# Kernel optimization log

Measured on AMD Instinct MI355X. Metric: run time of the kernel, lower is better.

Reference implementation:

```python
import jax, jax.numpy as jnp
import numpy as np

B, S, D = 2, 2048, 1024
H, E = 16, 64


def setup_inputs() -> dict:
    key = jax.random.key(0)
    k1, k2, k3, k4 = jax.random.split(key, 4)
    x = jax.random.normal(k1, (B, S, D), dtype=jnp.float32)
    # per-head Q/K/V projection weights, stacked over the head axis
    scale = 1.0 / np.sqrt(D)
    Wq = jax.random.normal(k2, (H, D, E), dtype=jnp.float32) * scale
    Wk = jax.random.normal(k3, (H, D, E), dtype=jnp.float32) * scale
    Wv = jax.random.normal(k4, (H, D, E), dtype=jnp.float32) * scale
    return {"x": x, "Wq": Wq, "Wk": Wk, "Wv": Wv}


def reference(x, Wq, Wk, Wv):
    # Grouped-over-heads equivalent of the per-head torch loop.
    q = jnp.einsum("bsd,hde->bhse", x, Wq)  # [B,H,S,E]
    k = jnp.einsum("bsd,hde->bhse", x, Wk)
    v = jnp.einsum("bsd,hde->bhse", x, Wv)

    scores = jnp.einsum("bhse,bhte->bhst", q, k)  # [B,H,S,S]
    scores = scores / jnp.sqrt(jnp.asarray(E, dtype=scores.dtype))
    causal = jnp.tril(jnp.ones((S, S), dtype=bool))  # True on/below diagonal
    scores = jnp.where(causal, scores, jnp.finfo(scores.dtype).min)
    attn = jax.nn.softmax(scores, axis=-1)  # dropout p=0.0 -> identity

    out = jnp.einsum("bhst,bhte->bhse", attn, v)  # [B,H,S,E]
    # concat over heads on the last dim, matching torch.concat(..., dim=-1)
    return out.transpose(0, 2, 1, 3).reshape(B, S, H * E)
```

## Files before the change

### kernel.cpp

```cpp
#include <hip/hip_runtime.h>
#include <stdint.h>

#define S_LEN 2048
#define D_DIM 1024
#define NB 2
#define NH 16
#define NE 64
#define M_ROWS (NB * S_LEN)
#define N_COLS (3 * NH * NE)
#define K_DIM D_DIM

typedef unsigned short u16;
typedef unsigned int u32;
typedef u16 u16x8 __attribute__((ext_vector_type(8)));
typedef __bf16 bf16x8 __attribute__((ext_vector_type(8)));
typedef float f32x4 __attribute__((ext_vector_type(4)));

__device__ __forceinline__ u16 f2b(float f) {
  u32 u = __builtin_bit_cast(u32, f);
  return (u16)((u + 0x7FFFu + ((u >> 16) & 1u)) >> 16);
}

__device__ __forceinline__ void gload_lds16(const void* g, void* l) {
  __builtin_amdgcn_global_load_lds(
      (const __attribute__((address_space(1))) u32*)g,
      (__attribute__((address_space(3))) u32*)l, 16, 0, 0);
}

__global__ __launch_bounds__(256) void k_prep_x(const float* __restrict__ x,
                                                u16* __restrict__ xb) {
  size_t t = (size_t)blockIdx.x * 256 + threadIdx.x;
  const float4* xf = (const float4*)x;
  float4 a = xf[2 * t], c = xf[2 * t + 1];
  u16x8 o;
  o[0] = f2b(a.x); o[1] = f2b(a.y); o[2] = f2b(a.z); o[3] = f2b(a.w);
  o[4] = f2b(c.x); o[5] = f2b(c.y); o[6] = f2b(c.z); o[7] = f2b(c.w);
  *(u16x8*)(xb + 8 * t) = o;
}

__global__ __launch_bounds__(256) void k_prep_w(const float* __restrict__ Wq,
                                                const float* __restrict__ Wk,
                                                const float* __restrict__ Wv,
                                                u16* __restrict__ Wt) {
  __shared__ u16 tile[64][65];
  int bid = blockIdx.x;
  int kb = bid & 15;
  int h = (bid >> 4) & 15;
  int proj = bid >> 8;
  const float* W = (proj == 0) ? Wq : ((proj == 1) ? Wk : Wv);
  int k0 = kb * 64;
  int t = threadIdx.x;
  int e = t & 63, kr = t >> 6;
  const float* src = W + ((size_t)h * D_DIM + k0 + kr * 16) * NE + e;
#pragma unroll
  for (int j = 0; j < 16; ++j) tile[kr * 16 + j][e] = f2b(src[(size_t)j * NE]);
  __syncthreads();
  int e2 = t >> 2, kc = (t & 3) * 16;
  u16x8 o0, o1;
#pragma unroll
  for (int j = 0; j < 8; ++j) { o0[j] = tile[kc + j][e2]; o1[j] = tile[kc + 8 + j][e2]; }
  size_t n = (size_t)proj * 1024 + h * 64 + e2;
  u16* dst = Wt + n * K_DIM + k0 + kc;
  *(u16x8*)dst = o0;
  *(u16x8*)(dst + 8) = o1;
}

__global__ __launch_bounds__(256) void k_gemm(const u16* __restrict__ A,
                                              const u16* __restrict__ Bt,
                                              u16* __restrict__ C) {
  __shared__ __align__(16) u16 As[128 * 64];
  __shared__ __align__(16) u16 Bs[128 * 64];
  int t = threadIdx.x;
  int lane = t & 63, w = t >> 6;
  int wr = (w >> 1) * 64, wc = (w & 1) * 64;
  int m0 = blockIdx.x * 128, n0 = blockIdx.y * 128;
  float qscale = ((n0 + wc) < 1024) ? 0.18033688f : 1.0f;
  f32x4 acc[4][4];
#pragma unroll
  for (int m = 0; m < 4; m++)
#pragma unroll
    for (int n = 0; n < 4; n++)
#pragma unroll
      for (int j = 0; j < 4; j++) acc[m][n][j] = 0.f;

  for (int k0 = 0; k0 < K_DIM; k0 += 64) {
#pragma unroll
    for (int i = 0; i < 4; ++i) {
      int ci = i * 256 + t;
      int row = ci >> 3, c = ci & 7;
      int cs = c ^ (row & 7);
      gload_lds16(A + (size_t)(m0 + row) * K_DIM + k0 + cs * 8,
                  (char*)As + (size_t)(i * 256 + w * 64) * 16);
      gload_lds16(Bt + (size_t)(n0 + row) * K_DIM + k0 + cs * 8,
                  (char*)Bs + (size_t)(i * 256 + w * 64) * 16);
    }
    __syncthreads();
#pragma unroll
    for (int ks = 0; ks < 2; ++ks) {
      int kc = ks * 4 + (lane >> 4);
      bf16x8 af[4], bfr[4];
#pragma unroll
      for (int m = 0; m < 4; m++) {
        int r = wr + m * 16 + (lane & 15);
        af[m] = *(const bf16x8*)&As[r * 64 + ((kc ^ (r & 7)) * 8)];
      }
#pragma unroll
      for (int n = 0; n < 4; n++) {
        int r = wc + n * 16 + (lane & 15);
        bfr[n] = *(const bf16x8*)&Bs[r * 64 + ((kc ^ (r & 7)) * 8)];
      }
#pragma unroll
      for (int m = 0; m < 4; m++)
#pragma unroll
        for (int n = 0; n < 4; n++)
          acc[m][n] = __builtin_amdgcn_mfma_f32_16x16x32_bf16(af[m], bfr[n], acc[m][n], 0, 0, 0);
    }
    __syncthreads();
  }
#pragma unroll
  for (int m = 0; m < 4; m++) {
#pragma unroll
    for (int r = 0; r < 4; r++) {
      int row = m0 + wr + m * 16 + (lane >> 4) * 4 + r;
#pragma unroll
      for (int n = 0; n < 4; n++) {
        int col = n0 + wc + n * 16 + (lane & 15);
        C[(size_t)row * N_COLS + col] = f2b(acc[m][n][r] * qscale);
      }
    }
  }
}

__device__ __forceinline__ void stage_k(const u16* kb_, u16* kdst, int kv0, int t, int w) {
#pragma unroll
  for (int i = 0; i < 2; ++i) {
    int ci = i * 256 + t;
    int row = ci >> 3, c = ci & 7;
    int cs = c ^ (row & 7);
    gload_lds16(kb_ + (size_t)(kv0 + row) * N_COLS + cs * 8,
                (char*)kdst + (size_t)(i * 256 + w * 64) * 16);
  }
}

__device__ __forceinline__ void vwrite(u16* vt, u16x8 va, u16x8 vb2, int vp, int vec) {
#pragma unroll
  for (int j = 0; j < 8; ++j) {
    int e = vec * 8 + j;
    int slot = (vp >> 2) ^ (e & 7) ^ (e >> 3);
    *(u32*)((char*)vt + e * 128 + slot * 16 + (vp & 3) * 4) =
        (u32)va[j] | ((u32)vb2[j] << 16);
  }
}

__global__ __launch_bounds__(256) void k_attn(const u16* __restrict__ qkv,
                                              float* __restrict__ out) {
  __shared__ __align__(16) u16 Ks[2][64 * 64];
  __shared__ __align__(16) u16 Vt[2][64 * 64];
  __shared__ __align__(16) u16 Ps[64 * 64];
  int t = threadIdx.x;
  int lane = t & 63, w = t >> 6;
  int bid = blockIdx.x;
  int x = bid & 7, g = bid >> 3;
  int bh = x * 4 + (g & 3);
  int qt = 31 - (g >> 2);
  int b = bh >> 4, h = bh & 15;
  const u16* qb_ = qkv + (size_t)b * S_LEN * N_COLS + h * NE;
  const u16* kb_ = qb_ + 1024;
  const u16* vb_ = qb_ + 2048;
  int vp = t >> 3, vec = t & 7;

  int q0 = qt * 64;
  int nt = qt + 1;

  int qrow = q0 + w * 16 + (lane & 15);
  bf16x8 qf[2];
#pragma unroll
  for (int ks = 0; ks < 2; ks++)
    qf[ks] = *(const bf16x8*)(qb_ + (size_t)qrow * N_COLS + ks * 32 + (lane >> 4) * 8);

  f32x4 o[4];
#pragma unroll
  for (int i = 0; i < 4; i++)
#pragma unroll
    for (int j = 0; j < 4; j++) o[i][j] = 0.f;
  float lrow[4];
#pragma unroll
  for (int r = 0; r < 4; r++) lrow[r] = 0.f;
  int myq = q0 + w * 16 + (lane >> 4) * 4;

  stage_k(kb_, Ks[0], 0, t, w);
  {
    const u16* vs = vb_ + (size_t)(2 * vp) * N_COLS + vec * 8;
    u16x8 va = *(const u16x8*)vs;
    u16x8 vb2 = *(const u16x8*)(vs + N_COLS);
    vwrite(Vt[0], va, vb2, vp, vec);
  }
  __syncthreads();

  int cur = 0;
  for (int ti = 0; ti < nt; ++ti) {
    int kv0 = ti * 64;
    bool pf = (ti + 1 < nt);
    u16x8 va, vb2;
    if (pf) {
      const u16* vs = vb_ + (size_t)(kv0 + 64 + 2 * vp) * N_COLS + vec * 8;
      va = *(const u16x8*)vs;
      vb2 = *(const u16x8*)(vs + N_COLS);
      stage_k(kb_, Ks[cur ^ 1], kv0 + 64, t, w);
    }

    f32x4 s[4];
#pragma unroll
    for (int f = 0; f < 4; f++)
#pragma unroll
      for (int j = 0; j < 4; j++) s[f][j] = 0.f;
    __builtin_amdgcn_s_setprio(1);
#pragma unroll
    for (int ks = 0; ks < 2; ks++) {
      int kc = ks * 4 + (lane >> 4);
#pragma unroll
      for (int f = 0; f < 4; f++) {
        int r = f * 16 + (lane & 15);
        bf16x8 kf = *(const bf16x8*)&Ks[cur][r * 64 + ((kc ^ (r & 7)) * 8)];
        s[f] = __builtin_amdgcn_mfma_f32_16x16x32_bf16(qf[ks], kf, s[f], 0, 0, 0);
      }
    }
    __builtin_amdgcn_s_setprio(0);

    bool diag = (ti == nt - 1);
#pragma unroll
    for (int r = 0; r < 4; ++r) {
#pragma unroll
      for (int f = 0; f < 4; f++) {
        float p = __builtin_amdgcn_exp2f(s[f][r]);
        if (diag) {
          int kv = kv0 + f * 16 + (lane & 15);
          p = (kv <= myq + r) ? p : 0.f;
        }
        s[f][r] = p;
      }
      lrow[r] += (s[0][r] + s[1][r]) + (s[2][r] + s[3][r]);
    }

#pragma unroll
    for (int f = 0; f < 4; f++) {
#pragma unroll
      for (int r = 0; r < 4; r++) {
        int row = w * 16 + (lane >> 4) * 4 + r;
        int col = f * 16 + (lane & 15);
        int swz = (col >> 3) ^ (row & 7);
        *(u16*)((char*)Ps + row * 128 + swz * 16 + (col & 7) * 2) =
            __builtin_bit_cast(u16, (__bf16)s[f][r]);
      }
    }

    if (pf) vwrite(Vt[cur ^ 1], va, vb2, vp, vec);

    __builtin_amdgcn_s_setprio(1);
#pragma unroll
    for (int ks = 0; ks < 2; ks++) {
      int kc = ks * 4 + (lane >> 4);
      int pr = w * 16 + (lane & 15);
      bf16x8 pa = *(const bf16x8*)&Ps[pr * 64 + ((kc ^ (pr & 7)) * 8)];
#pragma unroll
      for (int ef = 0; ef < 4; ef++) {
        int vr = ef * 16 + (lane & 15);
        int vswz = kc ^ (vr & 7) ^ (vr >> 3);
        bf16x8 vbf = *(const bf16x8*)&Vt[cur][vr * 64 + vswz * 8];
        o[ef] = __builtin_amdgcn_mfma_f32_16x16x32_bf16(pa, vbf, o[ef], 0, 0, 0);
      }
    }
    __builtin_amdgcn_s_setprio(0);
    __syncthreads();
    cur ^= 1;
  }

#pragma unroll
  for (int r = 0; r < 4; r++) {
    float l = lrow[r];
    l += __shfl_xor(l, 1);
    l += __shfl_xor(l, 2);
    l += __shfl_xor(l, 4);
    l += __shfl_xor(l, 8);
    float inv = 1.0f / l;
    int q = myq + r;
#pragma unroll
    for (int ef = 0; ef < 4; ef++) {
      int col = h * NE + ef * 16 + (lane & 15);
      out[((size_t)b * S_LEN + q) * (NH * NE) + col] = o[ef][r] * inv;
    }
  }
}

extern "C" void kernel_launch(void* const* d_in, const int* in_sizes, int n_in,
                              void* d_out, int out_size, void* d_ws, size_t ws_size,
                              hipStream_t stream) {
  const float* x = (const float*)d_in[0];
  const float* Wq = (const float*)d_in[1];
  const float* Wk = (const float*)d_in[2];
  const float* Wv = (const float*)d_in[3];
  float* out = (float*)d_out;

  char* ws = (char*)d_ws;
  u16* xb = (u16*)ws;
  u16* Wt = (u16*)(ws + (8u << 20));
  u16* qkv = (u16*)(ws + (14u << 20));

  k_prep_x<<<dim3(2048), dim3(256), 0, stream>>>(x, xb);
  k_prep_w<<<dim3(768), dim3(256), 0, stream>>>(Wq, Wk, Wv, Wt);
  k_gemm<<<dim3(32, 24), dim3(256), 0, stream>>>(xb, Wt, qkv);
  k_attn<<<dim3(1024), dim3(256), 0, stream>>>(qkv, out);
}
```

Baseline: 98.19 us.

## Merge prep kernels, remap GEMM blocks per XCD, use 128-row query tiles

Merges the x and weight conversion kernels into one launch to remove a kernel boundary. Remaps the GEMM grid to 1D so each XCD works on a contiguous group of column tiles, aiming for better L2 reuse of the weights. The attention kernel grows to 512 threads with 128 query rows per block, so each K/V tile staged in shared memory serves twice as many queries. Only the first 256 threads load V, and the last two KV tiles are masked. This halves the attention grid and may lower occupancy or leave load imbalance across the causal blocks.

Measured after the change: 100.3 us. +2.1%, slower.

```diff
diff --git a/kernel.cpp b/kernel.cpp
--- a/kernel.cpp
+++ b/kernel.cpp
@@ -27,42 +27,44 @@
       (__attribute__((address_space(3))) u32*)l, 16, 0, 0);
 }
 
-__global__ __launch_bounds__(256) void k_prep_x(const float* __restrict__ x,
-                                                u16* __restrict__ xb) {
-  size_t t = (size_t)blockIdx.x * 256 + threadIdx.x;
-  const float4* xf = (const float4*)x;
-  float4 a = xf[2 * t], c = xf[2 * t + 1];
-  u16x8 o;
-  o[0] = f2b(a.x); o[1] = f2b(a.y); o[2] = f2b(a.z); o[3] = f2b(a.w);
-  o[4] = f2b(c.x); o[5] = f2b(c.y); o[6] = f2b(c.z); o[7] = f2b(c.w);
-  *(u16x8*)(xb + 8 * t) = o;
-}
-
-__global__ __launch_bounds__(256) void k_prep_w(const float* __restrict__ Wq,
-                                                const float* __restrict__ Wk,
-                                                const float* __restrict__ Wv,
-                                                u16* __restrict__ Wt) {
+__global__ __launch_bounds__(256) void k_prep(const float* __restrict__ x,
+                                              const float* __restrict__ Wq,
+                                              const float* __restrict__ Wk,
+                                              const float* __restrict__ Wv,
+                                              u16* __restrict__ xb,
+                                              u16* __restrict__ Wt) {
   __shared__ u16 tile[64][65];
   int bid = blockIdx.x;
-  int kb = bid & 15;
-  int h = (bid >> 4) & 15;
-  int proj = bid >> 8;
-  const float* W = (proj == 0) ? Wq : ((proj == 1) ? Wk : Wv);
-  int k0 = kb * 64;
   int t = threadIdx.x;
-  int e = t & 63, kr = t >> 6;
-  const float* src = W + ((size_t)h * D_DIM + k0 + kr * 16) * NE + e;
-#pragma unroll
-  for (int j = 0; j < 16; ++j) tile[kr * 16 + j][e] = f2b(src[(size_t)j * NE]);
-  __syncthreads();
-  int e2 = t >> 2, kc = (t & 3) * 16;
-  u16x8 o0, o1;
-#pragma unroll
-  for (int j = 0; j < 8; ++j) { o0[j] = tile[kc + j][e2]; o1[j] = tile[kc + 8 + j][e2]; }
-  size_t n = (size_t)proj * 1024 + h * 64 + e2;
-  u16* dst = Wt + n * K_DIM + k0 + kc;
-  *(u16x8*)dst = o0;
-  *(u16x8*)(dst + 8) = o1;
+  if (bid < 2048) {
+    size_t i = (size_t)bid * 256 + t;
+    const float4* xf = (const float4*)x;
+    float4 a = xf[2 * i], c = xf[2 * i + 1];
+    u16x8 o;
+    o[0] = f2b(a.x); o[1] = f2b(a.y); o[2] = f2b(a.z); o[3] = f2b(a.w);
+    o[4] = f2b(c.x); o[5] = f2b(c.y); o[6] = f2b(c.z); o[7] = f2b(c.w);
+    *(u16x8*)(xb + 8 * i) = o;
+  } else {
+    int wbid = bid - 2048;
+    int kb = wbid & 15;
+    int h = (wbid >> 4) & 15;
+    int proj = wbid >> 8;
+    const float* W = (proj == 0) ? Wq : ((proj == 1) ? Wk : Wv);
+    int k0 = kb * 64;
+    int e = t & 63, kr = t >> 6;
+    const float* src = W + ((size_t)h * D_DIM + k0 + kr * 16) * NE + e;
+#pragma unroll
+    for (int j = 0; j < 16; ++j) tile[kr * 16 + j][e] = f2b(src[(size_t)j * NE]);
+    __syncthreads();
+    int e2 = t >> 2, kc = (t & 3) * 16;
+    u16x8 o0, o1;
+#pragma unroll
+    for (int j = 0; j < 8; ++j) { o0[j] = tile[kc + j][e2]; o1[j] = tile[kc + 8 + j][e2]; }
+    size_t n = (size_t)proj * 1024 + h * 64 + e2;
+    u16* dst = Wt + n * K_DIM + k0 + kc;
+    *(u16x8*)dst = o0;
+    *(u16x8*)(dst + 8) = o1;
+  }
 }
 
 __global__ __launch_bounds__(256) void k_gemm(const u16* __restrict__ A,
@@ -73,7 +75,10 @@
   int t = threadIdx.x;
   int lane = t & 63, w = t >> 6;
   int wr = (w >> 1) * 64, wc = (w & 1) * 64;
-  int m0 = blockIdx.x * 128, n0 = blockIdx.y * 128;
+  int bid = blockIdx.x;
+  int xcd = bid & 7, r0 = bid >> 3;
+  int m0 = (r0 / 3) * 128;
+  int n0 = (xcd * 3 + (r0 % 3)) * 128;
   float qscale = ((n0 + wc) < 1024) ? 0.18033688f : 1.0f;
   f32x4 acc[4][4];
 #pragma unroll
@@ -131,15 +136,11 @@
   }
 }
 
-__device__ __forceinline__ void stage_k(const u16* kb_, u16* kdst, int kv0, int t, int w) {
-#pragma unroll
-  for (int i = 0; i < 2; ++i) {
-    int ci = i * 256 + t;
-    int row = ci >> 3, c = ci & 7;
-    int cs = c ^ (row & 7);
-    gload_lds16(kb_ + (size_t)(kv0 + row) * N_COLS + cs * 8,
-                (char*)kdst + (size_t)(i * 256 + w * 64) * 16);
-  }
+__device__ __forceinline__ void stage_k(const u16* kb_, u16* kdst, int kv0, int t) {
+  int row = t >> 3, c = t & 7;
+  int cs = c ^ (row & 7);
+  gload_lds16(kb_ + (size_t)(kv0 + row) * N_COLS + cs * 8,
+              (char*)kdst + (size_t)t * 16);
 }
 
 __device__ __forceinline__ void vwrite(u16* vt, u16x8 va, u16x8 vb2, int vp, int vec) {
@@ -152,25 +153,25 @@
   }
 }
 
-__global__ __launch_bounds__(256) void k_attn(const u16* __restrict__ qkv,
+__global__ __launch_bounds__(512) void k_attn(const u16* __restrict__ qkv,
                                               float* __restrict__ out) {
   __shared__ __align__(16) u16 Ks[2][64 * 64];
   __shared__ __align__(16) u16 Vt[2][64 * 64];
-  __shared__ __align__(16) u16 Ps[64 * 64];
+  __shared__ __align__(16) u16 Ps[128 * 64];
   int t = threadIdx.x;
   int lane = t & 63, w = t >> 6;
   int bid = blockIdx.x;
-  int x = bid & 7, g = bid >> 3;
-  int bh = x * 4 + (g & 3);
-  int qt = 31 - (g >> 2);
+  int xcd = bid & 7, g = bid >> 3;
+  int bh = xcd * 4 + (g & 3);
+  int qb = 15 - (g >> 2);
   int b = bh >> 4, h = bh & 15;
   const u16* qb_ = qkv + (size_t)b * S_LEN * N_COLS + h * NE;
   const u16* kb_ = qb_ + 1024;
   const u16* vb_ = qb_ + 2048;
   int vp = t >> 3, vec = t & 7;
 
-  int q0 = qt * 64;
-  int nt = qt + 1;
+  int q0 = qb * 128;
+  int nt = 2 * qb + 2;
 
   int qrow = q0 + w * 16 + (lane & 15);
   bf16x8 qf[2];
@@ -188,8 +189,8 @@
   for (int r = 0; r < 4; r++) lrow[r] = 0.f;
   int myq = q0 + w * 16 + (lane >> 4) * 4;
 
-  stage_k(kb_, Ks[0], 0, t, w);
-  {
+  stage_k(kb_, Ks[0], 0, t);
+  if (t < 256) {
     const u16* vs = vb_ + (size_t)(2 * vp) * N_COLS + vec * 8;
     u16x8 va = *(const u16x8*)vs;
     u16x8 vb2 = *(const u16x8*)(vs + N_COLS);
@@ -203,10 +204,12 @@
     bool pf = (ti + 1 < nt);
     u16x8 va, vb2;
     if (pf) {
-      const u16* vs = vb_ + (size_t)(kv0 + 64 + 2 * vp) * N_COLS + vec * 8;
-      va = *(const u16x8*)vs;
-      vb2 = *(const u16x8*)(vs + N_COLS);
-      stage_k(kb_, Ks[cur ^ 1], kv0 + 64, t, w);
+      if (t < 256) {
+        const u16* vs = vb_ + (size_t)(kv0 + 64 + 2 * vp) * N_COLS + vec * 8;
+        va = *(const u16x8*)vs;
+        vb2 = *(const u16x8*)(vs + N_COLS);
+      }
+      stage_k(kb_, Ks[cur ^ 1], kv0 + 64, t);
     }
 
     f32x4 s[4];
@@ -227,13 +230,13 @@
     }
     __builtin_amdgcn_s_setprio(0);
 
-    bool diag = (ti == nt - 1);
+    bool mask = (ti >= nt - 2);
 #pragma unroll
     for (int r = 0; r < 4; ++r) {
 #pragma unroll
       for (int f = 0; f < 4; f++) {
         float p = __builtin_amdgcn_exp2f(s[f][r]);
-        if (diag) {
+        if (mask) {
           int kv = kv0 + f * 16 + (lane & 15);
           p = (kv <= myq + r) ? p : 0.f;
         }
@@ -254,7 +257,7 @@
       }
     }
 
-    if (pf) vwrite(Vt[cur ^ 1], va, vb2, vp, vec);
+    if (pf && t < 256) vwrite(Vt[cur ^ 1], va, vb2, vp, vec);
 
     __builtin_amdgcn_s_setprio(1);
 #pragma unroll
@@ -306,8 +309,7 @@
   u16* Wt = (u16*)(ws + (8u << 20));
   u16* qkv = (u16*)(ws + (14u << 20));
 
-  k_prep_x<<<dim3(2048), dim3(256), 0, stream>>>(x, xb);
-  k_prep_w<<<dim3(768), dim3(256), 0, stream>>>(Wq, Wk, Wv, Wt);
-  k_gemm<<<dim3(32, 24), dim3(256), 0, stream>>>(xb, Wt, qkv);
-  k_attn<<<dim3(1024), dim3(256), 0, stream>>>(qkv, out);
-}
+  k_prep<<<dim3(2816), dim3(256), 0, stream>>>(x, Wq, Wk, Wv, xb, Wt);
+  k_gemm<<<dim3(768), dim3(256), 0, stream>>>(xb, Wt, qkv);
+  k_attn<<<dim3(512), dim3(512), 0, stream>>>(qkv, out);
+}
```

## Merge prep kernels, remap GEMM blocks per XCD, keep P in registers

Applied to the files above, without the earlier changes.

Combines the x-conversion and weight-transpose kernels into one launch, which removes one kernel launch. Remaps GEMM blocks to a 1D grid so each XCD gets a contiguous set of N tiles, aiming for better L2 reuse. In attention it swaps the MFMA operand order so S comes out transposed, which lets P feed the PV MFMA straight from registers without the shared-memory round trip. The V fragments are then read as two 8-byte LDS loads, and the row-sum reduction changes to match. The extra LDS reads for V and the shuffle-based normalisation add some cost.

Measured after the change: 93.92 us. 1.05x faster.

```diff
diff --git a/kernel.cpp b/kernel.cpp
--- a/kernel.cpp
+++ b/kernel.cpp
@@ -6,7 +6,6 @@
 #define NB 2
 #define NH 16
 #define NE 64
-#define M_ROWS (NB * S_LEN)
 #define N_COLS (3 * NH * NE)
 #define K_DIM D_DIM
 
@@ -14,6 +13,7 @@
 typedef unsigned int u32;
 typedef u16 u16x8 __attribute__((ext_vector_type(8)));
 typedef __bf16 bf16x8 __attribute__((ext_vector_type(8)));
+typedef __bf16 bf16x4 __attribute__((ext_vector_type(4)));
 typedef float f32x4 __attribute__((ext_vector_type(4)));
 
 __device__ __forceinline__ u16 f2b(float f) {
@@ -27,42 +27,44 @@
       (__attribute__((address_space(3))) u32*)l, 16, 0, 0);
 }
 
-__global__ __launch_bounds__(256) void k_prep_x(const float* __restrict__ x,
-                                                u16* __restrict__ xb) {
-  size_t t = (size_t)blockIdx.x * 256 + threadIdx.x;
-  const float4* xf = (const float4*)x;
-  float4 a = xf[2 * t], c = xf[2 * t + 1];
-  u16x8 o;
-  o[0] = f2b(a.x); o[1] = f2b(a.y); o[2] = f2b(a.z); o[3] = f2b(a.w);
-  o[4] = f2b(c.x); o[5] = f2b(c.y); o[6] = f2b(c.z); o[7] = f2b(c.w);
-  *(u16x8*)(xb + 8 * t) = o;
-}
-
-__global__ __launch_bounds__(256) void k_prep_w(const float* __restrict__ Wq,
-                                                const float* __restrict__ Wk,
-                                                const float* __restrict__ Wv,
-                                                u16* __restrict__ Wt) {
+__global__ __launch_bounds__(256) void k_prep(const float* __restrict__ x,
+                                              const float* __restrict__ Wq,
+                                              const float* __restrict__ Wk,
+                                              const float* __restrict__ Wv,
+                                              u16* __restrict__ xb,
+                                              u16* __restrict__ Wt) {
   __shared__ u16 tile[64][65];
   int bid = blockIdx.x;
-  int kb = bid & 15;
-  int h = (bid >> 4) & 15;
-  int proj = bid >> 8;
-  const float* W = (proj == 0) ? Wq : ((proj == 1) ? Wk : Wv);
-  int k0 = kb * 64;
   int t = threadIdx.x;
-  int e = t & 63, kr = t >> 6;
-  const float* src = W + ((size_t)h * D_DIM + k0 + kr * 16) * NE + e;
-#pragma unroll
-  for (int j = 0; j < 16; ++j) tile[kr * 16 + j][e] = f2b(src[(size_t)j * NE]);
-  __syncthreads();
-  int e2 = t >> 2, kc = (t & 3) * 16;
-  u16x8 o0, o1;
-#pragma unroll
-  for (int j = 0; j < 8; ++j) { o0[j] = tile[kc + j][e2]; o1[j] = tile[kc + 8 + j][e2]; }
-  size_t n = (size_t)proj * 1024 + h * 64 + e2;
-  u16* dst = Wt + n * K_DIM + k0 + kc;
-  *(u16x8*)dst = o0;
-  *(u16x8*)(dst + 8) = o1;
+  if (bid < 2048) {
+    size_t i = (size_t)bid * 256 + t;
+    const float4* xf = (const float4*)x;
+    float4 a = xf[2 * i], c = xf[2 * i + 1];
+    u16x8 o;
+    o[0] = f2b(a.x); o[1] = f2b(a.y); o[2] = f2b(a.z); o[3] = f2b(a.w);
+    o[4] = f2b(c.x); o[5] = f2b(c.y); o[6] = f2b(c.z); o[7] = f2b(c.w);
+    *(u16x8*)(xb + 8 * i) = o;
+  } else {
+    int wbid = bid - 2048;
+    int kb = wbid & 15;
+    int h = (wbid >> 4) & 15;
+    int proj = wbid >> 8;
+    const float* W = (proj == 0) ? Wq : ((proj == 1) ? Wk : Wv);
+    int k0 = kb * 64;
+    int e = t & 63, kr = t >> 6;
+    const float* src = W + ((size_t)h * D_DIM + k0 + kr * 16) * NE + e;
+#pragma unroll
+    for (int j = 0; j < 16; ++j) tile[kr * 16 + j][e] = f2b(src[(size_t)j * NE]);
+    __syncthreads();
+    int e2 = t >> 2, kc = (t & 3) * 16;
+    u16x8 o0, o1;
+#pragma unroll
+    for (int j = 0; j < 8; ++j) { o0[j] = tile[kc + j][e2]; o1[j] = tile[kc + 8 + j][e2]; }
+    size_t n = (size_t)proj * 1024 + h * 64 + e2;
+    u16* dst = Wt + n * K_DIM + k0 + kc;
+    *(u16x8*)dst = o0;
+    *(u16x8*)(dst + 8) = o1;
+  }
 }
 
 __global__ __launch_bounds__(256) void k_gemm(const u16* __restrict__ A,
@@ -73,7 +75,10 @@
   int t = threadIdx.x;
   int lane = t & 63, w = t >> 6;
   int wr = (w >> 1) * 64, wc = (w & 1) * 64;
-  int m0 = blockIdx.x * 128, n0 = blockIdx.y * 128;
+  int bid = blockIdx.x;
+  int xcd = bid & 7, r0 = bid >> 3;
+  int m0 = (r0 / 3) * 128;
+  int n0 = (xcd * 3 + (r0 % 3)) * 128;
   float qscale = ((n0 + wc) < 1024) ? 0.18033688f : 1.0f;
   f32x4 acc[4][4];
 #pragma unroll
@@ -156,9 +161,9 @@
                                               float* __restrict__ out) {
   __shared__ __align__(16) u16 Ks[2][64 * 64];
   __shared__ __align__(16) u16 Vt[2][64 * 64];
-  __shared__ __align__(16) u16 Ps[64 * 64];
   int t = threadIdx.x;
   int lane = t & 63, w = t >> 6;
+  int hi = lane >> 4, l15 = lane & 15;
   int bid = blockIdx.x;
   int x = bid & 7, g = bid >> 3;
   int bh = x * 4 + (g & 3);
@@ -171,22 +176,20 @@
 
   int q0 = qt * 64;
   int nt = qt + 1;
-
-  int qrow = q0 + w * 16 + (lane & 15);
+  int wqb = q0 + w * 16;
+
   bf16x8 qf[2];
 #pragma unroll
   for (int ks = 0; ks < 2; ks++)
-    qf[ks] = *(const bf16x8*)(qb_ + (size_t)qrow * N_COLS + ks * 32 + (lane >> 4) * 8);
+    qf[ks] = *(const bf16x8*)(qb_ + (size_t)(wqb + l15) * N_COLS + ks * 32 + hi * 8);
 
   f32x4 o[4];
 #pragma unroll
   for (int i = 0; i < 4; i++)
 #pragma unroll
     for (int j = 0; j < 4; j++) o[i][j] = 0.f;
-  float lrow[4];
-#pragma unroll
-  for (int r = 0; r < 4; r++) lrow[r] = 0.f;
-  int myq = q0 + w * 16 + (lane >> 4) * 4;
+  float lsum = 0.f;
+  int myq = wqb + l15;
 
   stage_k(kb_, Ks[0], 0, t, w);
   {
@@ -217,40 +220,28 @@
     __builtin_amdgcn_s_setprio(1);
 #pragma unroll
     for (int ks = 0; ks < 2; ks++) {
-      int kc = ks * 4 + (lane >> 4);
+      int kc = ks * 4 + hi;
 #pragma unroll
       for (int f = 0; f < 4; f++) {
-        int r = f * 16 + (lane & 15);
+        int r = f * 16 + l15;
         bf16x8 kf = *(const bf16x8*)&Ks[cur][r * 64 + ((kc ^ (r & 7)) * 8)];
-        s[f] = __builtin_amdgcn_mfma_f32_16x16x32_bf16(qf[ks], kf, s[f], 0, 0, 0);
+        s[f] = __builtin_amdgcn_mfma_f32_16x16x32_bf16(kf, qf[ks], s[f], 0, 0, 0);
       }
     }
     __builtin_amdgcn_s_setprio(0);
 
     bool diag = (ti == nt - 1);
 #pragma unroll
-    for (int r = 0; r < 4; ++r) {
-#pragma unroll
-      for (int f = 0; f < 4; f++) {
+    for (int f = 0; f < 4; f++) {
+#pragma unroll
+      for (int r = 0; r < 4; r++) {
         float p = __builtin_amdgcn_exp2f(s[f][r]);
         if (diag) {
-          int kv = kv0 + f * 16 + (lane & 15);
-          p = (kv <= myq + r) ? p : 0.f;
+          int kv = kv0 + f * 16 + 4 * hi + r;
+          p = (kv <= myq) ? p : 0.f;
         }
         s[f][r] = p;
-      }
-      lrow[r] += (s[0][r] + s[1][r]) + (s[2][r] + s[3][r]);
-    }
-
-#pragma unroll
-    for (int f = 0; f < 4; f++) {
-#pragma unroll
-      for (int r = 0; r < 4; r++) {
-        int row = w * 16 + (lane >> 4) * 4 + r;
-        int col = f * 16 + (lane & 15);
-        int swz = (col >> 3) ^ (row & 7);
-        *(u16*)((char*)Ps + row * 128 + swz * 16 + (col & 7) * 2) =
-            __builtin_bit_cast(u16, (__bf16)s[f][r]);
+        lsum += p;
       }
     }
 
@@ -259,14 +250,25 @@
     __builtin_amdgcn_s_setprio(1);
 #pragma unroll
     for (int ks = 0; ks < 2; ks++) {
-      int kc = ks * 4 + (lane >> 4);
-      int pr = w * 16 + (lane & 15);
-      bf16x8 pa = *(const bf16x8*)&Ps[pr * 64 + ((kc ^ (pr & 7)) * 8)];
+      bf16x8 pa;
+#pragma unroll
+      for (int j = 0; j < 4; j++) {
+        pa[j] = (__bf16)s[2 * ks][j];
+        pa[4 + j] = (__bf16)s[2 * ks + 1][j];
+      }
+      int kvo1 = 32 * ks + 4 * hi;
+      int kvo2 = kvo1 + 16;
 #pragma unroll
       for (int ef = 0; ef < 4; ef++) {
-        int vr = ef * 16 + (lane & 15);
-        int vswz = kc ^ (vr & 7) ^ (vr >> 3);
-        bf16x8 vbf = *(const bf16x8*)&Vt[cur][vr * 64 + vswz * 8];
+        int e = ef * 16 + l15;
+        int sw = (e & 7) ^ (e >> 3);
+        int a1 = e * 128 + (((kvo1 >> 3) ^ sw) * 16) + (kvo1 & 7) * 2;
+        int a2 = e * 128 + (((kvo2 >> 3) ^ sw) * 16) + (kvo2 & 7) * 2;
+        bf16x4 vlo = *(const bf16x4*)((const char*)Vt[cur] + a1);
+        bf16x4 vhi = *(const bf16x4*)((const char*)Vt[cur] + a2);
+        bf16x8 vbf;
+#pragma unroll
+        for (int j = 0; j < 4; j++) { vbf[j] = vlo[j]; vbf[4 + j] = vhi[j]; }
         o[ef] = __builtin_amdgcn_mfma_f32_16x16x32_bf16(pa, vbf, o[ef], 0, 0, 0);
       }
     }
@@ -275,18 +277,16 @@
     cur ^= 1;
   }
 
+  lsum += __shfl_xor(lsum, 16);
+  lsum += __shfl_xor(lsum, 32);
 #pragma unroll
   for (int r = 0; r < 4; r++) {
-    float l = lrow[r];
-    l += __shfl_xor(l, 1);
-    l += __shfl_xor(l, 2);
-    l += __shfl_xor(l, 4);
-    l += __shfl_xor(l, 8);
+    float l = __shfl(lsum, 4 * hi + r);
     float inv = 1.0f / l;
-    int q = myq + r;
+    int q = wqb + 4 * hi + r;
 #pragma unroll
     for (int ef = 0; ef < 4; ef++) {
-      int col = h * NE + ef * 16 + (lane & 15);
+      int col = h * NE + ef * 16 + l15;
       out[((size_t)b * S_LEN + q) * (NH * NE) + col] = o[ef][r] * inv;
     }
   }
@@ -306,8 +306,7 @@
   u16* Wt = (u16*)(ws + (8u << 20));
   u16* qkv = (u16*)(ws + (14u << 20));
 
-  k_prep_x<<<dim3(2048), dim3(256), 0, stream>>>(x, xb);
-  k_prep_w<<<dim3(768), dim3(256), 0, stream>>>(Wq, Wk, Wv, Wt);
-  k_gemm<<<dim3(32, 24), dim3(256), 0, stream>>>(xb, Wt, qkv);
+  k_prep<<<dim3(2816), dim3(256), 0, stream>>>(x, Wq, Wk, Wv, xb, Wt);
+  k_gemm<<<dim3(768), dim3(256), 0, stream>>>(xb, Wt, qkv);
   k_attn<<<dim3(1024), dim3(256), 0, stream>>>(qkv, out);
 }
```
